# Optimization experiments

Measured on AMD Instinct MI355X. Metric: run time of the kernel, lower is better.

Reference implementation:

```python
import jax, jax.numpy as jnp
import numpy as np

B, NQ, NKV, D = 2, 2048, 2048, 1024
N_HEADS = 16
D_H = D // N_HEADS


def setup_inputs() -> dict:
    key = jax.random.key(0)
    ks = jax.random.split(key, 10)
    s = 0.02  # weight init scale
    return {
        "q": jax.random.normal(ks[0], (B, NQ, D), jnp.float32),
        "kv": jax.random.normal(ks[1], (B, NKV, D), jnp.float32),
        "Wq": jax.random.normal(ks[2], (D, D), jnp.float32) * s,
        "bq": jnp.zeros((D,), jnp.float32),
        "Wk": jax.random.normal(ks[3], (D, D), jnp.float32) * s,
        "bk": jnp.zeros((D,), jnp.float32),
        "Wv": jax.random.normal(ks[4], (D, D), jnp.float32) * s,
        "bv": jnp.zeros((D,), jnp.float32),
        "Wo": jax.random.normal(ks[5], (D, D), jnp.float32) * s,
        "bo": jnp.zeros((D,), jnp.float32),
    }


def reference(q, kv, Wq, bq, Wk, bk, Wv, bv, Wo, bo):
    # Linear projections (torch Linear: x @ W.T + b)
    qh = q @ Wq.T + bq   # [B, NQ, D]
    kh = kv @ Wk.T + bk  # [B, NKV, D]
    vh = kv @ Wv.T + bv  # [B, NKV, D]
    # Split heads: [B, N, H, d_h]
    qh = qh.reshape(B, NQ, N_HEADS, D_H)
    kh = kh.reshape(B, NKV, N_HEADS, D_H)
    vh = vh.reshape(B, NKV, N_HEADS, D_H)
    scale = 1.0 / jnp.sqrt(jnp.asarray(D_H, qh.dtype))
    # QK^T per head: [B, H, NQ, NKV]
    scores = jnp.einsum("bqhd,bkhd->bhqk", qh, kh) * scale
    att = jax.nn.softmax(scores, axis=-1)
    # dropout p=0.0 -> identity
    out = jnp.einsum("bhqk,bkhd->bqhd", att, vh)  # [B, NQ, H, d_h]
    out = out.reshape(B, NQ, D)
    return out @ Wo.T + bo
```

## Files before the change

### kernel.cpp

```cpp
#include <hip/hip_runtime.h>
#include <cstddef>
#include <cstdint>

using half4v  = __attribute__((ext_vector_type(4))) _Float16;
using half8   = __attribute__((ext_vector_type(8))) _Float16;
using floatx4 = __attribute__((ext_vector_type(4))) float;

#define B_   2
#define NQ_  2048
#define DM   1024
#define NH_  16
#define DH_  64
#define NTILES 32

__device__ __forceinline__ void async16(const _Float16* g, _Float16* l) {
    __builtin_amdgcn_global_load_lds(
        (const __attribute__((address_space(1))) unsigned int*)g,
        (__attribute__((address_space(3))) unsigned int*)l, 16, 0, 0);
}

__global__ __launch_bounds__(256) void cvt_all(
        const float* __restrict__ q,  const float* __restrict__ kv,
        const float* __restrict__ wq, const float* __restrict__ wk,
        const float* __restrict__ wv, const float* __restrict__ wo,
        _Float16* __restrict__ dq,  _Float16* __restrict__ dkv,
        _Float16* __restrict__ dwq, _Float16* __restrict__ dwk,
        _Float16* __restrict__ dwv, _Float16* __restrict__ dwo) {
    int blk = blockIdx.x;
    const float* s;
    _Float16* d;
    int base;
    if (blk < 2048)      { s = q;  d = dq;  base = blk; }
    else if (blk < 4096) { s = kv; d = dkv; base = blk - 2048; }
    else if (blk < 4608) { s = wq; d = dwq; base = blk - 4096; }
    else if (blk < 5120) { s = wk; d = dwk; base = blk - 4608; }
    else if (blk < 5632) { s = wv; d = dwv; base = blk - 5120; }
    else                 { s = wo; d = dwo; base = blk - 5632; }
    int i = base * 256 + threadIdx.x;
    const float4* s4 = (const float4*)s;
    float4 a = s4[2 * i], b = s4[2 * i + 1];
    half8 h;
    h[0] = (_Float16)a.x; h[1] = (_Float16)a.y; h[2] = (_Float16)a.z; h[3] = (_Float16)a.w;
    h[4] = (_Float16)b.x; h[5] = (_Float16)b.y; h[6] = (_Float16)b.z; h[7] = (_Float16)b.w;
    ((half8*)d)[i] = h;
}

__global__ __launch_bounds__(256, 3) void proj_qkv(
        const _Float16* __restrict__ q16, const _Float16* __restrict__ kv16,
        const _Float16* __restrict__ wqp, const _Float16* __restrict__ wkp,
        const _Float16* __restrict__ wvp,
        const float* __restrict__ bqp, const float* __restrict__ bkp,
        const float* __restrict__ bvp,
        _Float16* __restrict__ qh, _Float16* __restrict__ kh,
        _Float16* __restrict__ vt) {
    __shared__ _Float16 As[128 * 64];
    __shared__ _Float16 Bs[128 * 64];

    const int which = blockIdx.x >> 8;
    const int sub = blockIdx.x & 255;
    const _Float16* A = (which == 0) ? q16 : kv16;
    const _Float16* W = (which == 0) ? wqp : (which == 1) ? wkp : wvp;
    const float* bias = (which == 0) ? bqp : (which == 1) ? bkp : bvp;

    const int t = threadIdx.x;
    const int w = t >> 6, lane = t & 63;
    const int r16 = lane & 15, quad = lane >> 4;
    const int bm = (sub & 7) * 4 + ((sub >> 3) & 3);
    const int bn = sub >> 5;
    const int m0 = bm * 128, n0 = bn * 128;
    const int wm = w >> 1, wn = w & 1;

    floatx4 acc[4][4];
#pragma unroll
    for (int i = 0; i < 4; i++)
#pragma unroll
        for (int j = 0; j < 4; j++)
#pragma unroll
            for (int r = 0; r < 4; r++) acc[i][j][r] = 0.f;

    const int ph0 = quad ^ (r16 & 7), ph1 = ph0 ^ 4;

    for (int k0 = 0; k0 < DM; k0 += 64) {
        __syncthreads();
#pragma unroll
        for (int i = 0; i < 4; i++) {
            int P = i * 256 + t;
            int m = P >> 3, c = (P & 7) ^ (m & 7);
            async16(A + (size_t)(m0 + m) * DM + k0 + c * 8, &As[P * 8]);
            async16(W + (size_t)(n0 + m) * DM + k0 + c * 8, &Bs[P * 8]);
        }
        asm volatile("s_waitcnt vmcnt(0)" ::: "memory");
        __syncthreads();

        half8 af[4][2], bf[4][2];
#pragma unroll
        for (int mi = 0; mi < 4; mi++) {
            int m = wm * 64 + mi * 16 + r16;
            af[mi][0] = ((const half8*)As)[m * 8 + ph0];
            af[mi][1] = ((const half8*)As)[m * 8 + ph1];
        }
#pragma unroll
        for (int ni = 0; ni < 4; ni++) {
            int n = wn * 64 + ni * 16 + r16;
            bf[ni][0] = ((const half8*)Bs)[n * 8 + ph0];
            bf[ni][1] = ((const half8*)Bs)[n * 8 + ph1];
        }
#pragma unroll
        for (int kd = 0; kd < 2; kd++)
#pragma unroll
            for (int mi = 0; mi < 4; mi++)
#pragma unroll
                for (int ni = 0; ni < 4; ni++)
                    acc[mi][ni] = __builtin_amdgcn_mfma_f32_16x16x32_f16(
                        af[mi][kd], bf[ni][kd], acc[mi][ni], 0, 0, 0);
    }

    if (which < 2) {
        _Float16* C = (which == 0) ? qh : kh;
        const float esc = (which == 0) ? 0.125f : 1.0f;
#pragma unroll
        for (int mi = 0; mi < 4; mi++)
#pragma unroll
            for (int r = 0; r < 4; r++) {
                int row = m0 + wm * 64 + mi * 16 + quad * 4 + r;
#pragma unroll
                for (int ni = 0; ni < 4; ni++) {
                    int col = n0 + wn * 64 + ni * 16 + r16;
                    C[(size_t)row * DM + col] = (_Float16)((acc[mi][ni][r] + bias[col]) * esc);
                }
            }
    } else {
#pragma unroll
        for (int mi = 0; mi < 4; mi++) {
            int krow = m0 + wm * 64 + mi * 16 + quad * 4;
            int bb = krow >> 11, kk = krow & 2047;
#pragma unroll
            for (int ni = 0; ni < 4; ni++) {
                int col = n0 + wn * 64 + ni * 16 + r16;
                int hh = col >> 6, dd = col & 63;
                float bv = bias[col];
                half4v pk;
#pragma unroll
                for (int r = 0; r < 4; r++) pk[r] = (_Float16)(acc[mi][ni][r] + bv);
                *(half4v*)&vt[((size_t)((bb * NH_ + hh) * DH_ + dd)) * NQ_ + kk] = pk;
            }
        }
    }
}

__global__ __launch_bounds__(256, 4) void attn_mfma(const _Float16* __restrict__ Qg,
                                                    const _Float16* __restrict__ Kg,
                                                    const _Float16* __restrict__ Vt,
                                                    _Float16* __restrict__ Og) {
    __shared__ _Float16 Ps[64 * 64];
    __shared__ _Float16 Ks[2][64 * 64];
    __shared__ _Float16 Vs[2][64 * 64];

    const int t = threadIdx.x, w = t >> 6, lane = t & 63;
    const int r16 = lane & 15, quad = lane >> 4;
    const int blk = blockIdx.x;
    const int bh = (blk & 7) * 4 + ((blk >> 3) & 3);
    const int qt = blk >> 5;
    const int b = bh >> 4, h = bh & 15;

    const _Float16* qbase = Qg + (size_t)(b * NQ_ + qt * 64) * DM + h * DH_;
    const _Float16* kbase = Kg + (size_t)(b * NQ_) * DM + h * DH_;
    const _Float16* vbase = Vt + (size_t)bh * DH_ * NQ_;

#pragma unroll
    for (int i = 0; i < 2; i++) {
        int P = i * 256 + t;
        int m = P >> 3, c = (P & 7) ^ (m & 7);
        async16(qbase + (size_t)m * DM + c * 8, &Ps[P * 8]);
        async16(kbase + (size_t)m * DM + c * 8, &Ks[0][P * 8]);
        async16(vbase + (size_t)m * NQ_ + c * 8, &Vs[0][P * 8]);
    }
    asm volatile("s_waitcnt vmcnt(0)" ::: "memory");
    __syncthreads();

    const int ph0 = quad ^ (r16 & 7), ph1 = ph0 ^ 4;
    half8 Qf[2];
    {
        int m = w * 16 + r16;
        Qf[0] = ((const half8*)Ps)[m * 8 + ph0];
        Qf[1] = ((const half8*)Ps)[m * 8 + ph1];
    }

    floatx4 oaccT[4];
    float lacc = 0.f;
#pragma unroll
    for (int nd = 0; nd < 4; nd++)
#pragma unroll
        for (int r = 0; r < 4; r++) oaccT[nd][r] = 0.f;

    for (int kt = 0; kt < NTILES; kt++) {
        const int cur = kt & 1;
        asm volatile("s_waitcnt vmcnt(0)" ::: "memory");
        __syncthreads();

        if (kt + 1 < NTILES) {
            const int nxt = cur ^ 1;
#pragma unroll
            for (int i = 0; i < 2; i++) {
                int P = i * 256 + t;
                int m = P >> 3, c = (P & 7) ^ (m & 7);
                async16(kbase + (size_t)((kt + 1) * 64 + m) * DM + c * 8, &Ks[nxt][P * 8]);
                async16(vbase + (size_t)m * NQ_ + (kt + 1) * 64 + c * 8, &Vs[nxt][P * 8]);
            }
        }

        floatx4 sacc[4];
#pragma unroll
        for (int nk = 0; nk < 4; nk++)
#pragma unroll
            for (int r = 0; r < 4; r++) sacc[nk][r] = 0.f;
#pragma unroll
        for (int kd = 0; kd < 2; kd++)
#pragma unroll
            for (int nk = 0; nk < 4; nk++) {
                half8 kf = ((const half8*)Ks[cur])[(nk * 16 + r16) * 8 + (kd ? ph1 : ph0)];
                sacc[nk] = __builtin_amdgcn_mfma_f32_16x16x32_f16(kf, Qf[kd], sacc[nk], 0, 0, 0);
            }

        const int q = w * 16 + r16;
#pragma unroll
        for (int nk = 0; nk < 4; nk++) {
            float p0 = __expf(sacc[nk][0]);
            float p1 = __expf(sacc[nk][1]);
            float p2 = __expf(sacc[nk][2]);
            float p3 = __expf(sacc[nk][3]);
            lacc += (p0 + p1) + (p2 + p3);
            half4v pk;
            pk[0] = (_Float16)p0; pk[1] = (_Float16)p1;
            pk[2] = (_Float16)p2; pk[3] = (_Float16)p3;
            int phys = (nk * 2 + (quad >> 1)) ^ (r16 & 7);
            *(half4v*)&Ps[q * 64 + phys * 8 + (quad & 1) * 4] = pk;
        }

#pragma unroll
        for (int ks = 0; ks < 2; ks++) {
            half8 pf = ((const half8*)Ps)[q * 8 + ((ks * 4 + quad) ^ (r16 & 7))];
#pragma unroll
            for (int nd = 0; nd < 4; nd++) {
                half8 vf = ((const half8*)Vs[cur])[(nd * 16 + r16) * 8 + ((ks * 4 + quad) ^ (r16 & 7))];
                oaccT[nd] = __builtin_amdgcn_mfma_f32_16x16x32_f16(vf, pf, oaccT[nd], 0, 0, 0);
            }
        }
    }

    {
        float l = lacc;
        l += __shfl_xor(l, 16);
        l += __shfl_xor(l, 32);
        float inv = 1.f / l;
        int qrow = b * NQ_ + qt * 64 + w * 16 + r16;
#pragma unroll
        for (int nd = 0; nd < 4; nd++) {
            half4v o;
#pragma unroll
            for (int r = 0; r < 4; r++) o[r] = (_Float16)(oaccT[nd][r] * inv);
            *(half4v*)&Og[(size_t)qrow * DM + h * DH_ + nd * 16 + quad * 4] = o;
        }
    }
}

__global__ __launch_bounds__(256, 4) void gemm_o(const _Float16* __restrict__ A,
                                                 const _Float16* __restrict__ W,
                                                 const float* __restrict__ bias,
                                                 float* __restrict__ C) {
    __shared__ _Float16 As[64 * 64];
    __shared__ _Float16 Bs[64 * 64];

    const int t = threadIdx.x;
    const int w = t >> 6, lane = t & 63;
    const int r16 = lane & 15, quad = lane >> 4;
    const int blk = blockIdx.x;
    const int bm = (blk & 7) * 8 + ((blk >> 3) & 7);
    const int bn = blk >> 6;
    const int m0 = bm * 64, n0 = bn * 64;
    const int wm = w >> 1, wn = w & 1;

    floatx4 acc[2][2];
#pragma unroll
    for (int i = 0; i < 2; i++)
#pragma unroll
        for (int j = 0; j < 2; j++)
#pragma unroll
            for (int r = 0; r < 4; r++) acc[i][j][r] = 0.f;

    const int ph0 = quad ^ (r16 & 7), ph1 = ph0 ^ 4;

    for (int k0 = 0; k0 < DM; k0 += 64) {
        __syncthreads();
#pragma unroll
        for (int i = 0; i < 2; i++) {
            int P = i * 256 + t;
            int m = P >> 3, c = (P & 7) ^ (m & 7);
            async16(A + (size_t)(m0 + m) * DM + k0 + c * 8, &As[P * 8]);
            async16(W + (size_t)(n0 + m) * DM + k0 + c * 8, &Bs[P * 8]);
        }
        asm volatile("s_waitcnt vmcnt(0)" ::: "memory");
        __syncthreads();

        half8 af[2][2], bf[2][2];
#pragma unroll
        for (int mi = 0; mi < 2; mi++) {
            int m = wm * 32 + mi * 16 + r16;
            af[mi][0] = ((const half8*)As)[m * 8 + ph0];
            af[mi][1] = ((const half8*)As)[m * 8 + ph1];
        }
#pragma unroll
        for (int ni = 0; ni < 2; ni++) {
            int n = wn * 32 + ni * 16 + r16;
            bf[ni][0] = ((const half8*)Bs)[n * 8 + ph0];
            bf[ni][1] = ((const half8*)Bs)[n * 8 + ph1];
        }
#pragma unroll
        for (int kd = 0; kd < 2; kd++)
#pragma unroll
            for (int mi = 0; mi < 2; mi++)
#pragma unroll
                for (int ni = 0; ni < 2; ni++)
                    acc[mi][ni] = __builtin_amdgcn_mfma_f32_16x16x32_f16(
                        af[mi][kd], bf[ni][kd], acc[mi][ni], 0, 0, 0);
    }

#pragma unroll
    for (int mi = 0; mi < 2; mi++)
#pragma unroll
        for (int r = 0; r < 4; r++) {
            int row = m0 + wm * 32 + mi * 16 + quad * 4 + r;
#pragma unroll
            for (int ni = 0; ni < 2; ni++) {
                int col = n0 + wn * 32 + ni * 16 + r16;
                C[(size_t)row * DM + col] = acc[mi][ni][r] + bias[col];
            }
        }
}

extern "C" void kernel_launch(void* const* d_in, const int* in_sizes, int n_in,
                              void* d_out, int out_size, void* d_ws, size_t ws_size,
                              hipStream_t stream) {
    const float* q  = (const float*)d_in[0];
    const float* kv = (const float*)d_in[1];
    const float* Wq = (const float*)d_in[2];
    const float* bq = (const float*)d_in[3];
    const float* Wk = (const float*)d_in[4];
    const float* bk = (const float*)d_in[5];
    const float* Wv = (const float*)d_in[6];
    const float* bv = (const float*)d_in[7];
    const float* Wo = (const float*)d_in[8];
    const float* bo = (const float*)d_in[9];

    char* ws = (char*)d_ws;
    _Float16* q16  = (_Float16*)(ws);
    _Float16* kv16 = (_Float16*)(ws + (size_t)(8  << 20));
    _Float16* w16q = (_Float16*)(ws + (size_t)(16 << 20));
    _Float16* w16k = (_Float16*)(ws + (size_t)(18 << 20));
    _Float16* w16v = (_Float16*)(ws + (size_t)(20 << 20));
    _Float16* w16o = (_Float16*)(ws + (size_t)(22 << 20));
    _Float16* qh16 = (_Float16*)(ws + (size_t)(24 << 20));
    _Float16* kh16 = (_Float16*)(ws + (size_t)(32 << 20));
    _Float16* vt16 = (_Float16*)(ws + (size_t)(40 << 20));
    _Float16* ao16 = (_Float16*)(ws + (size_t)(48 << 20));

    cvt_all<<<6144, 256, 0, stream>>>(q, kv, Wq, Wk, Wv, Wo,
                                      q16, kv16, w16q, w16k, w16v, w16o);

    proj_qkv<<<768, 256, 0, stream>>>(q16, kv16, w16q, w16k, w16v,
                                      bq, bk, bv, qh16, kh16, vt16);

    attn_mfma<<<1024, 256, 0, stream>>>(qh16, kh16, vt16, ao16);

    gemm_o<<<1024, 256, 0, stream>>>(ao16, w16o, bo, (float*)d_out);
}
```

Before: 198.6 us.

## Enlarge attention query tile to 128 rows with 2 waves of 64 rows each

```diff
diff --git a/kernel.cpp b/kernel.cpp
--- a/kernel.cpp
+++ b/kernel.cpp
@@ -148,11 +148,11 @@
     }
 }
 
-__global__ __launch_bounds__(256, 4) void attn_mfma(const _Float16* __restrict__ Qg,
+__global__ __launch_bounds__(128, 1) void attn_mfma(const _Float16* __restrict__ Qg,
                                                     const _Float16* __restrict__ Kg,
                                                     const _Float16* __restrict__ Vt,
                                                     _Float16* __restrict__ Og) {
-    __shared__ _Float16 Ps[64 * 64];
+    __shared__ _Float16 Ps[128 * 64];
     __shared__ _Float16 Ks[2][64 * 64];
     __shared__ _Float16 Vs[2][64 * 64];
 
@@ -163,35 +163,50 @@
     const int qt = blk >> 5;
     const int b = bh >> 4, h = bh & 15;
 
-    const _Float16* qbase = Qg + (size_t)(b * NQ_ + qt * 64) * DM + h * DH_;
+    const _Float16* qbase = Qg + (size_t)(b * NQ_ + qt * 128) * DM + h * DH_;
     const _Float16* kbase = Kg + (size_t)(b * NQ_) * DM + h * DH_;
     const _Float16* vbase = Vt + (size_t)bh * DH_ * NQ_;
 
 #pragma unroll
-    for (int i = 0; i < 2; i++) {
-        int P = i * 256 + t;
+    for (int i = 0; i < 8; i++) {
+        int P = i * 128 + t;
         int m = P >> 3, c = (P & 7) ^ (m & 7);
         async16(qbase + (size_t)m * DM + c * 8, &Ps[P * 8]);
+    }
+#pragma unroll
+    for (int i = 0; i < 4; i++) {
+        int P = i * 128 + t;
+        int m = P >> 3, c = (P & 7) ^ (m & 7);
         async16(kbase + (size_t)m * DM + c * 8, &Ks[0][P * 8]);
         async16(vbase + (size_t)m * NQ_ + c * 8, &Vs[0][P * 8]);
     }
     asm volatile("s_waitcnt vmcnt(0)" ::: "memory");
     __syncthreads();
 
-    const int ph0 = quad ^ (r16 & 7), ph1 = ph0 ^ 4;
-    half8 Qf[2];
-    {
-        int m = w * 16 + r16;
-        Qf[0] = ((const half8*)Ps)[m * 8 + ph0];
-        Qf[1] = ((const half8*)Ps)[m * 8 + ph1];
-    }
-
-    floatx4 oaccT[4];
-    float lacc = 0.f;
-#pragma unroll
-    for (int nd = 0; nd < 4; nd++)
-#pragma unroll
-        for (int r = 0; r < 4; r++) oaccT[nd][r] = 0.f;
+    half8 Qf[4][2];
+#pragma unroll
+    for (int qsub = 0; qsub < 4; qsub++) {
+        int ql = w * 64 + qsub * 16 + r16;
+#pragma unroll
+        for (int kd = 0; kd < 2; kd++)
+            Qf[qsub][kd] = ((const half8*)Ps)[ql * 8 + ((kd * 4 + quad) ^ (r16 & 7))];
+    }
+
+    half8 ones;
+#pragma unroll
+    for (int j = 0; j < 8; j++) ones[j] = (_Float16)1.0f;
+
+    floatx4 oaccT[4][4];
+    floatx4 lacc[4];
+#pragma unroll
+    for (int i = 0; i < 4; i++) {
+#pragma unroll
+        for (int r = 0; r < 4; r++) lacc[i][r] = 0.f;
+#pragma unroll
+        for (int j = 0; j < 4; j++)
+#pragma unroll
+            for (int r = 0; r < 4; r++) oaccT[i][j][r] = 0.f;
+    }
 
     for (int kt = 0; kt < NTILES; kt++) {
         const int cur = kt & 1;
@@ -201,65 +216,76 @@
         if (kt + 1 < NTILES) {
             const int nxt = cur ^ 1;
 #pragma unroll
-            for (int i = 0; i < 2; i++) {
-                int P = i * 256 + t;
+            for (int i = 0; i < 4; i++) {
+                int P = i * 128 + t;
                 int m = P >> 3, c = (P & 7) ^ (m & 7);
                 async16(kbase + (size_t)((kt + 1) * 64 + m) * DM + c * 8, &Ks[nxt][P * 8]);
                 async16(vbase + (size_t)m * NQ_ + (kt + 1) * 64 + c * 8, &Vs[nxt][P * 8]);
             }
         }
 
-        floatx4 sacc[4];
-#pragma unroll
-        for (int nk = 0; nk < 4; nk++)
-#pragma unroll
-            for (int r = 0; r < 4; r++) sacc[nk][r] = 0.f;
+        floatx4 sacc[4][4];
+#pragma unroll
+        for (int i = 0; i < 4; i++)
+#pragma unroll
+            for (int j = 0; j < 4; j++)
+#pragma unroll
+                for (int r = 0; r < 4; r++) sacc[i][j][r] = 0.f;
 #pragma unroll
         for (int kd = 0; kd < 2; kd++)
 #pragma unroll
-            for (int nk = 0; nk < 4; nk++) {
-                half8 kf = ((const half8*)Ks[cur])[(nk * 16 + r16) * 8 + (kd ? ph1 : ph0)];
-                sacc[nk] = __builtin_amdgcn_mfma_f32_16x16x32_f16(kf, Qf[kd], sacc[nk], 0, 0, 0);
-            }
-
-        const int q = w * 16 + r16;
-#pragma unroll
-        for (int nk = 0; nk < 4; nk++) {
-            float p0 = __expf(sacc[nk][0]);
-            float p1 = __expf(sacc[nk][1]);
-            float p2 = __expf(sacc[nk][2]);
-            float p3 = __expf(sacc[nk][3]);
-            lacc += (p0 + p1) + (p2 + p3);
-            half4v pk;
-            pk[0] = (_Float16)p0; pk[1] = (_Float16)p1;
-            pk[2] = (_Float16)p2; pk[3] = (_Float16)p3;
-            int phys = (nk * 2 + (quad >> 1)) ^ (r16 & 7);
-            *(half4v*)&Ps[q * 64 + phys * 8 + (quad & 1) * 4] = pk;
+            for (int ksub = 0; ksub < 4; ksub++) {
+                half8 kf = ((const half8*)Ks[cur])[(ksub * 16 + r16) * 8 + ((kd * 4 + quad) ^ (r16 & 7))];
+#pragma unroll
+                for (int qsub = 0; qsub < 4; qsub++)
+                    sacc[ksub][qsub] = __builtin_amdgcn_mfma_f32_16x16x32_f16(
+                        kf, Qf[qsub][kd], sacc[ksub][qsub], 0, 0, 0);
+            }
+
+#pragma unroll
+        for (int qsub = 0; qsub < 4; qsub++) {
+            int ql = w * 64 + qsub * 16 + r16;
+#pragma unroll
+            for (int ksub = 0; ksub < 4; ksub++) {
+                half4v pk;
+#pragma unroll
+                for (int r = 0; r < 4; r++) pk[r] = (_Float16)__expf(sacc[ksub][qsub][r]);
+                int phys = (ksub * 2 + (quad >> 1)) ^ (r16 & 7);
+                *(half4v*)&Ps[ql * 64 + phys * 8 + (quad & 1) * 4] = pk;
+            }
         }
 
 #pragma unroll
         for (int ks = 0; ks < 2; ks++) {
-            half8 pf = ((const half8*)Ps)[q * 8 + ((ks * 4 + quad) ^ (r16 & 7))];
-#pragma unroll
-            for (int nd = 0; nd < 4; nd++) {
-                half8 vf = ((const half8*)Vs[cur])[(nd * 16 + r16) * 8 + ((ks * 4 + quad) ^ (r16 & 7))];
-                oaccT[nd] = __builtin_amdgcn_mfma_f32_16x16x32_f16(vf, pf, oaccT[nd], 0, 0, 0);
-            }
-        }
-    }
-
-    {
-        float l = lacc;
-        l += __shfl_xor(l, 16);
-        l += __shfl_xor(l, 32);
-        float inv = 1.f / l;
-        int qrow = b * NQ_ + qt * 64 + w * 16 + r16;
-#pragma unroll
-        for (int nd = 0; nd < 4; nd++) {
+            half8 vf[4];
+#pragma unroll
+            for (int dsub = 0; dsub < 4; dsub++)
+                vf[dsub] = ((const half8*)Vs[cur])[(dsub * 16 + r16) * 8 + ((ks * 4 + quad) ^ (r16 & 7))];
+#pragma unroll
+            for (int qsub = 0; qsub < 4; qsub++) {
+                int ql = w * 64 + qsub * 16 + r16;
+                half8 pf = ((const half8*)Ps)[ql * 8 + ((ks * 4 + quad) ^ (r16 & 7))];
+                lacc[qsub] = __builtin_amdgcn_mfma_f32_16x16x32_f16(ones, pf, lacc[qsub], 0, 0, 0);
+#pragma unroll
+                for (int dsub = 0; dsub < 4; dsub++)
+                    oaccT[dsub][qsub] = __builtin_amdgcn_mfma_f32_16x16x32_f16(
+                        vf[dsub], pf, oaccT[dsub][qsub], 0, 0, 0);
+            }
+        }
+    }
+
+    float inv[4];
+#pragma unroll
+    for (int qsub = 0; qsub < 4; qsub++) inv[qsub] = 1.f / lacc[qsub][0];
+#pragma unroll
+    for (int qsub = 0; qsub < 4; qsub++) {
+        int qrow = b * NQ_ + qt * 128 + w * 64 + qsub * 16 + r16;
+#pragma unroll
+        for (int dsub = 0; dsub < 4; dsub++) {
             half4v o;
 #pragma unroll
-            for (int r = 0; r < 4; r++) o[r] = (_Float16)(oaccT[nd][r] * inv);
-            *(half4v*)&Og[(size_t)qrow * DM + h * DH_ + nd * 16 + quad * 4] = o;
+            for (int r = 0; r < 4; r++) o[r] = (_Float16)(oaccT[dsub][qsub][r] * inv[qsub]);
+            *(half4v*)&Og[(size_t)qrow * DM + h * DH_ + dsub * 16 + quad * 4] = o;
         }
     }
 }
@@ -370,7 +396,7 @@
     proj_qkv<<<768, 256, 0, stream>>>(q16, kv16, w16q, w16k, w16v,
                                       bq, bk, bv, qh16, kh16, vt16);
 
-    attn_mfma<<<1024, 256, 0, stream>>>(qh16, kh16, vt16, ao16);
+    attn_mfma<<<512, 128, 0, stream>>>(qh16, kh16, vt16, ao16);
 
     gemm_o<<<1024, 256, 0, stream>>>(ao16, w16o, bo, (float*)d_out);
 }
```

Result: slower. 219.0 us (+10.2%).
